# Kernel optimization log

Measured on AMD Instinct MI355X. Metric: run time of the kernel, lower is better.

The kernel has to match this reference:

```python
import jax, jax.numpy as jnp
import numpy as np

B, FAN_IN, FAN_OUT, K = 4096, 4096, 4096, 65536


def setup_inputs() -> dict:
    key = jax.random.key(0)
    k1, k2, k3 = jax.random.split(key, 3)
    a = jax.random.normal(k1, (B, FAN_IN), dtype=jnp.float32)
    # hash table H(i, j) -> bucket k in [0, K); replaces the python defaultdict hh
    hash_idx = jax.random.randint(k2, (FAN_OUT, FAN_IN + 1), 0, K)
    d = FAN_OUT * (FAN_IN + 1) / K  # matches d = fan_out * fan_in / K (fan_in already +1)
    W = jax.random.normal(k3, (K,), dtype=jnp.float32) / d
    return {"a": a, "hash_idx": hash_idx, "W": W}


def reference(a, hash_idx, W):
    # append bias column of ones: a_ext [B, fan_in+1]
    ones = jnp.ones((a.shape[0], 1), dtype=a.dtype)
    a_ext = jnp.concatenate([a, ones], axis=1)
    # virtual weight matrix via hash gather: Wv[i, j] = W[H(i, j)]
    Wv = W[hash_idx]  # [fan_out, fan_in+1]
    # out[b, i] = sum_j a_ext[b, j] * W[H(i, j)]
    # identical math to: a_kj[i,b,k] = sum_{j: H(i,j)=k} a_ext[b,j]; zz = a_kj @ W; zz.T
    return jnp.einsum('bj,ij->bi', a_ext, Wv)
```

## Files before the change

### kernel.cpp

```cpp
#include <hip/hip_runtime.h>
#include <hip/hip_bf16.h>
#include <stdint.h>


#define B_DIM   4096
#define FAN_IN  4096
#define FAN_OUT 4096
#define KD      (FAN_IN + 1)
#define KP      4160
#define NKT     65

#define BM 256
#define BN 256
#define BK 64

typedef __attribute__((ext_vector_type(8))) short  short8;
typedef __attribute__((ext_vector_type(4))) float  floatx4;

__device__ __forceinline__ unsigned short f2bf(float f) {
  union { float f; unsigned u; } v; v.f = f;
  unsigned u = v.u;
  u += 0x7fffu + ((u >> 16) & 1u);
  return (unsigned short)(u >> 16);
}

__device__ __forceinline__ void async16(const void* g, void* l) {
  __builtin_amdgcn_global_load_lds(
      (const __attribute__((address_space(1))) void*)g,
      (__attribute__((address_space(3))) void*)l, 16, 0, 0);
}

__global__ __launch_bounds__(256) void build_aext(
    const float* __restrict__ a, unsigned short* __restrict__ Ae) {
  const int row = blockIdx.x;
  const float* ar = a + (size_t)row * FAN_IN;
  unsigned short* er = Ae + (size_t)row * KP;
  for (int j4 = threadIdx.x; j4 < KP / 4; j4 += 256) {
    const int j = j4 * 4;
    float x0, x1, x2, x3;
    if (j + 3 < FAN_IN) {
      const float4 v = *(const float4*)(ar + j);
      x0 = v.x; x1 = v.y; x2 = v.z; x3 = v.w;
    } else {
      x0 = (j + 0 < FAN_IN) ? ar[j + 0] : ((j + 0 == FAN_IN) ? 1.0f : 0.0f);
      x1 = (j + 1 < FAN_IN) ? ar[j + 1] : ((j + 1 == FAN_IN) ? 1.0f : 0.0f);
      x2 = (j + 2 < FAN_IN) ? ar[j + 2] : ((j + 2 == FAN_IN) ? 1.0f : 0.0f);
      x3 = (j + 3 < FAN_IN) ? ar[j + 3] : ((j + 3 == FAN_IN) ? 1.0f : 0.0f);
    }
    ushort4 o;
    o.x = f2bf(x0); o.y = f2bf(x1); o.z = f2bf(x2); o.w = f2bf(x3);
    *(ushort4*)(er + j) = o;
  }
}

__global__ __launch_bounds__(512) void build_wv(
    const int* __restrict__ hidx, const float* __restrict__ W,
    unsigned short* __restrict__ Wv) {
  __shared__ unsigned short wl[32768];
  const int t  = threadIdx.x;
  const int r0 = blockIdx.x * 4;

  int          idx[4][9];
  unsigned short res[4][9];
#pragma unroll
  for (int row = 0; row < 4; row++) {
    const int* hr = hidx + (size_t)(r0 + row) * KD;
#pragma unroll
    for (int i = 0; i < 9; i++) {
      const int j = i * 512 + t;
      idx[row][i] = (j < KD) ? hr[j] : 0;
      res[row][i] = 0;
    }
  }

  for (int h = 0; h < 2; h++) {
    __syncthreads();
    const float4* Wb = (const float4*)(W + h * 32768);
#pragma unroll
    for (int i = 0; i < 16; i++) {
      const int f4 = i * 512 + t;
      const float4 v = Wb[f4];
      ushort4 o;
      o.x = f2bf(v.x); o.y = f2bf(v.y); o.z = f2bf(v.z); o.w = f2bf(v.w);
      *(ushort4*)&wl[f4 * 4] = o;
    }
    __syncthreads();
    const int lo = h << 15;
#pragma unroll
    for (int row = 0; row < 4; row++)
#pragma unroll
      for (int i = 0; i < 9; i++) {
        const int v = idx[row][i];
        if ((v & 32768) == lo)
          res[row][i] = wl[v & 32767];
      }
  }

#pragma unroll
  for (int row = 0; row < 4; row++) {
    unsigned short* wr = Wv + (size_t)(r0 + row) * KP;
#pragma unroll
    for (int i = 0; i < 9; i++) {
      const int j = i * 512 + t;
      if (j < KD) wr[j] = res[row][i];
    }
    if (t < KP - KD) wr[KD + t] = 0;
  }
}


#define STAGE_A(BUF, H, KOFF)                                                      \
  do {                                                                             \
    async16(pa + ((H) * 128 + 0)  * KP + (KOFF),                                   \
            smb + ((BUF) << 15) + ((H) << 14) + dA);                               \
    async16(pa + ((H) * 128 + 64) * KP + (KOFF),                                   \
            smb + ((BUF) << 15) + ((H) << 14) + 8192 + dA);                        \
  } while (0)

#define STAGE_B(BUF, H, KOFF)                                                      \
  do {                                                                             \
    async16(pb + ((H) * 128 + 0)  * KP + (KOFF),                                   \
            smb + 65536 + ((BUF) << 15) + ((H) << 14) + dA);                       \
    async16(pb + ((H) * 128 + 64) * KP + (KOFF),                                   \
            smb + 65536 + ((BUF) << 15) + ((H) << 14) + 8192 + dA);                \
  } while (0)

#define PHASE_MID()                                                                \
  do {                                                                             \
    asm volatile("" ::: "memory");                                                 \
    __builtin_amdgcn_s_barrier();                                                  \
    asm volatile("s_waitcnt lgkmcnt(0)" ::: "memory");                             \
    __builtin_amdgcn_sched_barrier(0);                                             \
    __builtin_amdgcn_s_setprio(1);                                                 \
  } while (0)

#define PHASE_END()                                                                \
  do {                                                                             \
    __builtin_amdgcn_s_setprio(0);                                                 \
    asm volatile("" ::: "memory");                                                 \
    __builtin_amdgcn_s_barrier();                                                  \
    asm volatile("" ::: "memory");                                                 \
  } while (0)

#define PHASE_END_TILE()                                                           \
  do {                                                                             \
    __builtin_amdgcn_s_setprio(0);                                                 \
    asm volatile("s_waitcnt vmcnt(4)" ::: "memory");                               \
    __builtin_amdgcn_s_barrier();                                                  \
    asm volatile("" ::: "memory");                                                 \
  } while (0)

#define MFMA2(ACC, AF, BF)                                                         \
  do {                                                                             \
    ACC = __builtin_amdgcn_mfma_f32_16x16x32_bf16((AF)[0], (BF)[0], ACC, 0, 0, 0); \
    ACC = __builtin_amdgcn_mfma_f32_16x16x32_bf16((AF)[1], (BF)[1], ACC, 0, 0, 0); \
  } while (0)

#define KTILE(P, K1, K2)                                                           \
  do {                                                                             \
    short8 af[4][2], bf[4][2];                                                     \
                       \
    _Pragma("unroll")                                                              \
    for (int mi = 0; mi < 4; ++mi) {                                               \
      af[mi][0] = *(const short8*)(smb + ((P) << 15) + arB + mi * 2048 + abase);   \
      af[mi][1] = *(const short8*)(smb + ((P) << 15) + arB + mi * 2048 + (abase ^ 64)); \
    }                                                                              \
    _Pragma("unroll")                                                              \
    for (int ni = 0; ni < 2; ++ni) {                                               \
      bf[ni][0] = *(const short8*)(smb + ((P) << 15) + brB + ni * 2048 + abase);   \
      bf[ni][1] = *(const short8*)(smb + ((P) << 15) + brB + ni * 2048 + (abase ^ 64)); \
    }                                                                              \
    STAGE_A((P) ^ 1, 1, K1);                                                       \
    PHASE_MID();                                                                   \
    _Pragma("unroll")                                                              \
    for (int mi = 0; mi < 4; ++mi)                                                 \
      _Pragma("unroll")                                                            \
      for (int ni = 0; ni < 2; ++ni) MFMA2(acc[mi][ni], af[mi], bf[ni]);           \
    PHASE_END();                                                                   \
               \
    _Pragma("unroll")                                                              \
    for (int ni = 2; ni < 4; ++ni) {                                               \
      bf[ni][0] = *(const short8*)(smb + ((P) << 15) + brB + ni * 2048 + abase);   \
      bf[ni][1] = *(const short8*)(smb + ((P) << 15) + brB + ni * 2048 + (abase ^ 64)); \
    }                                                                              \
    STAGE_B((P) ^ 1, 1, K1);                                                       \
    PHASE_MID();                                                                   \
    _Pragma("unroll")                                                              \
    for (int mi = 0; mi < 4; ++mi)                                                 \
      _Pragma("unroll")                                                            \
      for (int ni = 2; ni < 4; ++ni) MFMA2(acc[mi][ni], af[mi], bf[ni]);           \
    PHASE_END();                                                                   \
               \
            \
    _Pragma("unroll")                                                              \
    for (int mi = 0; mi < 4; ++mi) {                                               \
      af[mi][0] = *(const short8*)(smb + ((P) << 15) + arB + (mi + 4) * 2048 + abase); \
      af[mi][1] = *(const short8*)(smb + ((P) << 15) + arB + (mi + 4) * 2048 + (abase ^ 64)); \
    }                                                                              \
    STAGE_B((P), 0, K2);                                                           \
    PHASE_MID();                                                                   \
    _Pragma("unroll")                                                              \
    for (int mi = 0; mi < 4; ++mi)                                                 \
      _Pragma("unroll")                                                            \
      for (int ni = 0; ni < 2; ++ni) MFMA2(acc[mi + 4][ni], af[mi], bf[ni]);       \
    PHASE_END();                                                                   \
            \
            \
    STAGE_A((P), 0, K2);                                                           \
    PHASE_MID();                                                                   \
    _Pragma("unroll")                                                              \
    for (int mi = 0; mi < 4; ++mi)                                                 \
      _Pragma("unroll")                                                            \
      for (int ni = 2; ni < 4; ++ni) MFMA2(acc[mi + 4][ni], af[mi], bf[ni]);       \
    PHASE_END_TILE();       \
  } while (0)

__global__ __launch_bounds__(512, 2) void gemm_bt8(
    const unsigned short* __restrict__ A, const unsigned short* __restrict__ Bm,
    float* __restrict__ C, int M, int N) {
  extern __shared__ char smb[];
  const int tid = threadIdx.x;
  const int l   = tid & 63;
  const int w   = tid >> 6;
  const int wm  = w >> 2;
  const int wn  = w & 3;
  const int bm  = blockIdx.y * BM;
  const int bn  = blockIdx.x * BN;
  const int q   = l >> 4;
  const int r   = l & 15;

  const int lrow = l >> 3;
  const int lcol = ((l & 7) ^ lrow) * 8;
  const unsigned short* pa = A  + (size_t)(bm + w * 8 + lrow) * KP + lcol;
  const unsigned short* pb = Bm + (size_t)(bn + w * 8 + lrow) * KP + lcol;
  const int dA = w * 1024;

  const int abase = r * 128 + ((q ^ (r & 7)) << 4);
  const int arB   = wm << 14;
  const int brB   = 65536 + ((wn >> 1) << 14) + ((wn & 1) << 13);

  floatx4 acc[8][4] = {};

  STAGE_A(0, 0, 0); STAGE_A(0, 1, 0);
  STAGE_B(0, 0, 0); STAGE_B(0, 1, 0);
  STAGE_B(1, 0, 64); STAGE_A(1, 0, 64);
  asm volatile("s_waitcnt vmcnt(4)" ::: "memory");
  __builtin_amdgcn_s_barrier();
  asm volatile("" ::: "memory");

  int k1 = 64, k2 = 128;
#pragma unroll 1
  for (int tt = 0; tt < 32; ++tt) {
    const int k2c = (k2 > 4096) ? 4096 : k2;
    const int k3c = (k2 + 64 > 4096) ? 4096 : k2 + 64;
    KTILE(0, k1, k2c);
    KTILE(1, k2c, k3c);
    k1 += 128; k2 += 128;
  }

  {
    short8 af[8][2], bf[4][2];
#pragma unroll
    for (int mi = 0; mi < 8; ++mi) {
      af[mi][0] = *(const short8*)(smb + arB + mi * 2048 + abase);
      af[mi][1] = *(const short8*)(smb + arB + mi * 2048 + (abase ^ 64));
    }
#pragma unroll
    for (int ni = 0; ni < 4; ++ni) {
      bf[ni][0] = *(const short8*)(smb + brB + ni * 2048 + abase);
      bf[ni][1] = *(const short8*)(smb + brB + ni * 2048 + (abase ^ 64));
    }
    asm volatile("s_waitcnt lgkmcnt(0)" ::: "memory");
    __builtin_amdgcn_sched_barrier(0);
    __builtin_amdgcn_s_setprio(1);
#pragma unroll
    for (int mi = 0; mi < 8; ++mi)
#pragma unroll
      for (int ni = 0; ni < 4; ++ni) MFMA2(acc[mi][ni], af[mi], bf[ni]);
    __builtin_amdgcn_s_setprio(0);
  }

  asm volatile("s_waitcnt vmcnt(0)" ::: "memory");

  const int r0 = bm + wm * 128;
  const int c0 = bn + wn * 64;
#pragma unroll
  for (int mi = 0; mi < 8; ++mi)
#pragma unroll
    for (int ni = 0; ni < 4; ++ni) {
      const int row0 = r0 + mi * 16 + q * 4;
      const int col  = c0 + ni * 16 + r;
#pragma unroll
      for (int i = 0; i < 4; ++i)
        C[(size_t)(row0 + i) * N + col] = acc[mi][ni][i];
    }
}

extern "C" void kernel_launch(void* const* d_in, const int* in_sizes, int n_in,
                              void* d_out, int out_size, void* d_ws, size_t ws_size,
                              hipStream_t stream) {
  const float* a    = (const float*)d_in[0];
  const int*   hidx = (const int*)d_in[1];
  const float* W    = (const float*)d_in[2];
  float*       out  = (float*)d_out;

  unsigned short* Ae = (unsigned short*)d_ws;
  unsigned short* Wv = Ae + (size_t)B_DIM * KP;

  static bool attr_set = false;
  if (!attr_set) {
    hipFuncSetAttribute((const void*)gemm_bt8,
                        hipFuncAttributeMaxDynamicSharedMemorySize, 131072);
    attr_set = true;
  }

  build_aext<<<B_DIM, 256, 0, stream>>>(a, Ae);
  build_wv<<<FAN_OUT / 4, 512, 0, stream>>>(hidx, W, Wv);
  gemm_bt8<<<dim3(FAN_OUT / BN, B_DIM / BM), 512, 131072, stream>>>(Ae, Wv, out, B_DIM, FAN_OUT);
}
```

Baseline: 293.9 us.

## Load full bf16 weight table into LDS once and gather 16 rows per block

The hashed-weight gather kernel now holds the whole 64K-entry bf16 weight table in 128KB of dynamic LDS, so the two-pass half-table scheme and its extra syncs go away. Each block now handles 16 output rows instead of 4, which spreads the cost of loading and converting W over four times as many rows. Stores become ushort4 vectors. In exchange the block uses 1024 threads and 128KB of LDS, which limits occupancy to one block per CU, and the hash-index loads are scalar and strided by 4 across lanes.

```diff
diff --git a/kernel.cpp b/kernel.cpp
--- a/kernel.cpp
+++ b/kernel.cpp
@@ -53,58 +53,37 @@
   }
 }
 
-__global__ __launch_bounds__(512) void build_wv(
+__global__ __launch_bounds__(1024) void build_wv(
     const int* __restrict__ hidx, const float* __restrict__ W,
     unsigned short* __restrict__ Wv) {
-  __shared__ unsigned short wl[32768];
-  const int t  = threadIdx.x;
-  const int r0 = blockIdx.x * 4;
-
-  int          idx[4][9];
-  unsigned short res[4][9];
-#pragma unroll
-  for (int row = 0; row < 4; row++) {
-    const int* hr = hidx + (size_t)(r0 + row) * KD;
-#pragma unroll
-    for (int i = 0; i < 9; i++) {
-      const int j = i * 512 + t;
-      idx[row][i] = (j < KD) ? hr[j] : 0;
-      res[row][i] = 0;
-    }
-  }
-
-  for (int h = 0; h < 2; h++) {
-    __syncthreads();
-    const float4* Wb = (const float4*)(W + h * 32768);
-#pragma unroll
-    for (int i = 0; i < 16; i++) {
-      const int f4 = i * 512 + t;
-      const float4 v = Wb[f4];
-      ushort4 o;
-      o.x = f2bf(v.x); o.y = f2bf(v.y); o.z = f2bf(v.z); o.w = f2bf(v.w);
-      *(ushort4*)&wl[f4 * 4] = o;
-    }
-    __syncthreads();
-    const int lo = h << 15;
-#pragma unroll
-    for (int row = 0; row < 4; row++)
-#pragma unroll
-      for (int i = 0; i < 9; i++) {
-        const int v = idx[row][i];
-        if ((v & 32768) == lo)
-          res[row][i] = wl[v & 32767];
-      }
-  }
-
-#pragma unroll
-  for (int row = 0; row < 4; row++) {
-    unsigned short* wr = Wv + (size_t)(r0 + row) * KP;
-#pragma unroll
-    for (int i = 0; i < 9; i++) {
-      const int j = i * 512 + t;
-      if (j < KD) wr[j] = res[row][i];
-    }
-    if (t < KP - KD) wr[KD + t] = 0;
+  extern __shared__ unsigned short wl[];
+  const int t = threadIdx.x;
+
+  const float4* Wf = (const float4*)W;
+#pragma unroll
+  for (int i = 0; i < 16; i++) {
+    const int f4 = i * 1024 + t;
+    const float4 v = Wf[f4];
+    ushort4 o;
+    o.x = f2bf(v.x); o.y = f2bf(v.y); o.z = f2bf(v.z); o.w = f2bf(v.w);
+    *(ushort4*)&wl[f4 * 4] = o;
+  }
+  __syncthreads();
+
+  const int r0 = blockIdx.x * 16;
+#pragma unroll 4
+  for (int r = 0; r < 16; r++) {
+    const int* hr = hidx + (size_t)(r0 + r) * KD;
+    unsigned short* wr = Wv + (size_t)(r0 + r) * KP;
+    const int j = 4 * t;
+    ushort4 o;
+    o.x = wl[hr[j + 0]];
+    o.y = wl[hr[j + 1]];
+    o.z = wl[hr[j + 2]];
+    o.w = wl[hr[j + 3]];
+    *(ushort4*)(wr + j) = o;
+    if (t < 64)
+      wr[4096 + t] = (t == 0) ? wl[hr[4096]] : (unsigned short)0;
   }
 }
 
@@ -311,10 +290,12 @@
   if (!attr_set) {
     hipFuncSetAttribute((const void*)gemm_bt8,
                         hipFuncAttributeMaxDynamicSharedMemorySize, 131072);
+    hipFuncSetAttribute((const void*)build_wv,
+                        hipFuncAttributeMaxDynamicSharedMemorySize, 131072);
     attr_set = true;
   }
 
   build_aext<<<B_DIM, 256, 0, stream>>>(a, Ae);
-  build_wv<<<FAN_OUT / 4, 512, 0, stream>>>(hidx, W, Wv);
+  build_wv<<<FAN_OUT / 16, 1024, 131072, stream>>>(hidx, W, Wv);
   gemm_bt8<<<dim3(FAN_OUT / BN, B_DIM / BM), 512, 131072, stream>>>(Ae, Wv, out, B_DIM, FAN_OUT);
 }
```

New measurement: 285.0 us. -3.0%, faster.
